# Kernel tuning notes

Measured on AMD Instinct MI355X. Metric: run time of the kernel, lower is better.

## Reference

```python
import jax, jax.numpy as jnp
import numpy as np

HIDDEN = 512
NUM_HEADS = 8
HEAD = HIDDEN // NUM_HEADS
TOP_K = 64
NEG = -1e9


def setup_inputs() -> dict:
    key = jax.random.key(0)
    ks = jax.random.split(key, 12)
    B, Q, S = 2, 2048, 4096
    sc = 0.02
    return {
        "main_input": jax.random.normal(ks[0], (B, Q, HIDDEN), jnp.float32),
        "side_input": jax.random.normal(ks[1], (S, HIDDEN), jnp.float32),
        "att_mask": jax.random.randint(ks[2], (B, Q, S), 0, 2, jnp.int32),
        "Wq": jax.random.normal(ks[3], (HIDDEN, HIDDEN), jnp.float32) * sc,
        "bq": jnp.zeros((HIDDEN,), jnp.float32),
        "Wk": jax.random.normal(ks[4], (HIDDEN, HIDDEN), jnp.float32) * sc,
        "bk": jnp.zeros((HIDDEN,), jnp.float32),
        "Wv": jax.random.normal(ks[5], (HIDDEN, HIDDEN), jnp.float32) * sc,
        "bv": jnp.zeros((HIDDEN,), jnp.float32),
        "Wo": jax.random.normal(ks[6], (HIDDEN, HIDDEN), jnp.float32) * sc,
        "bo": jnp.zeros((HIDDEN,), jnp.float32),
    }


def reference(main_input, side_input, att_mask, Wq, bq, Wk, bk, Wv, bv, Wo, bo):
    B, Qlen, _ = main_input.shape
    S = side_input.shape[0]
    # multi-head projections; side K/V shared across the whole batch
    q = (main_input @ Wq + bq).reshape(B, Qlen, NUM_HEADS, HEAD)
    k = (side_input @ Wk + bk).reshape(S, NUM_HEADS, HEAD)
    v = (side_input @ Wv + bv).reshape(S, NUM_HEADS, HEAD)
    # scores: [B, H, Q, S]
    scores = jnp.einsum("bqhd,khd->bhqk", q, k) / jnp.sqrt(jnp.asarray(HEAD, q.dtype))
    # attention mask (0 = masked)
    mask = att_mask[:, None, :, :].astype(scores.dtype)  # [B,1,Q,S]
    scores = scores + (1.0 - mask) * NEG
    # top-k restriction: keep only the TOP_K largest scores per query row
    thresh = jax.lax.top_k(scores, TOP_K)[0][..., -1:]  # kth largest
    scores = jnp.where(scores >= thresh, scores, NEG)
    probs = jax.nn.softmax(scores, axis=-1)
    ctx = jnp.einsum("bhqk,khd->bqhd", probs, v).reshape(B, Qlen, HIDDEN)
    return ctx @ Wo + bo
```

## Files before the change

kernel.cpp:

```cpp
#include <hip/hip_runtime.h>
#include <stdint.h>

typedef uint32_t u32;
typedef unsigned long long u64;

#define NEGV (-1e9f)
#define NCAND 16
#define LISTCAP 256
#define RSCALE 2048.0f
#define RINV   (1.0f / 2048.0f)
#define DELTA  4e-3f

typedef __attribute__((ext_vector_type(8))) _Float16 half8;
typedef __attribute__((ext_vector_type(4))) float f32x4;

__device__ __forceinline__ u32 f2ord(float f) {
  u32 x = __float_as_uint(f);
  return (x & 0x80000000u) ? ~x : (x | 0x80000000u);
}
__device__ __forceinline__ float ord2f(u32 u) {
  u32 x = (u & 0x80000000u) ? (u ^ 0x80000000u) : ~u;
  return __uint_as_float(x);
}

__device__ __forceinline__ void gl_lds16(const unsigned short* g, unsigned short* l) {
  __builtin_amdgcn_global_load_lds(
      (const __attribute__((address_space(1))) u32*)g,
      (__attribute__((address_space(3))) u32*)l, 16, 0, 0);
}

__global__ __launch_bounds__(256)
void pack_mask(const int* __restrict__ mask, u64* __restrict__ mbits) {
  int w = blockIdx.x * 256 + threadIdx.x;
  const int4* p = (const int4*)(mask + (size_t)w * 64);
  u64 bits = 0;
#pragma unroll
  for (int j = 0; j < 16; ++j) {
    int4 m = p[j];
    if (m.x) bits |= 1ull << (j * 4 + 0);
    if (m.y) bits |= 1ull << (j * 4 + 1);
    if (m.z) bits |= 1ull << (j * 4 + 2);
    if (m.w) bits |= 1ull << (j * 4 + 3);
  }
  mbits[w] = bits;
}

__global__ __launch_bounds__(256)
void gemm_bias(const float* __restrict__ A, const float* __restrict__ W,
               const float* __restrict__ bias, float* __restrict__ C) {
  __shared__ float As[16][68];
  __shared__ float Bs[16][64];
  const int tid = threadIdx.x;
  const int tx = tid & 15, ty = tid >> 4;
  const int n0 = blockIdx.x << 6, m0 = blockIdx.y << 6;
  float c[4][4] = {};
  for (int k0 = 0; k0 < 512; k0 += 16) {
    {
      const int row = tid >> 2, kp = (tid & 3) << 2;
      float4 av = *(const float4*)&A[(size_t)(m0 + row) * 512 + k0 + kp];
      As[kp + 0][row] = av.x;
      As[kp + 1][row] = av.y;
      As[kp + 2][row] = av.z;
      As[kp + 3][row] = av.w;
      const int kk = tid >> 4, np = (tid & 15) << 2;
      *(float4*)&Bs[kk][np] = *(const float4*)&W[(size_t)(k0 + kk) * 512 + n0 + np];
    }
    __syncthreads();
#pragma unroll
    for (int kk = 0; kk < 16; ++kk) {
      float4 a = *(const float4*)&As[kk][ty << 2];
      float4 b = *(const float4*)&Bs[kk][tx << 2];
      c[0][0] += a.x * b.x; c[0][1] += a.x * b.y; c[0][2] += a.x * b.z; c[0][3] += a.x * b.w;
      c[1][0] += a.y * b.x; c[1][1] += a.y * b.y; c[1][2] += a.y * b.z; c[1][3] += a.y * b.w;
      c[2][0] += a.z * b.x; c[2][1] += a.z * b.y; c[2][2] += a.z * b.z; c[2][3] += a.z * b.w;
      c[3][0] += a.w * b.x; c[3][1] += a.w * b.y; c[3][2] += a.w * b.z; c[3][3] += a.w * b.w;
    }
    __syncthreads();
  }
  float4 bv = *(const float4*)&bias[n0 + (tx << 2)];
#pragma unroll
  for (int i = 0; i < 4; ++i) {
    float4 o;
    o.x = c[i][0] + bv.x; o.y = c[i][1] + bv.y;
    o.z = c[i][2] + bv.z; o.w = c[i][3] + bv.w;
    *(float4*)&C[(size_t)(m0 + (ty << 2) + i) * 512 + n0 + (tx << 2)] = o;
  }
}

__global__ __launch_bounds__(256)
void gemm_bias_split(const float* __restrict__ A, const float* __restrict__ W,
                     const float* __restrict__ bias,
                     unsigned short* __restrict__ Ph, unsigned short* __restrict__ Pl,
                     float* __restrict__ Pf, int qsh) {
  __shared__ float As[16][68];
  __shared__ float Bs[16][64];
  const int tid = threadIdx.x;
  const int tx = tid & 15, ty = tid >> 4;
  const int n0 = blockIdx.x << 6, m0 = blockIdx.y << 6;
  float c[4][4] = {};
  for (int k0 = 0; k0 < 512; k0 += 16) {
    {
      const int row = tid >> 2, kp = (tid & 3) << 2;
      float4 av = *(const float4*)&A[(size_t)(m0 + row) * 512 + k0 + kp];
      As[kp + 0][row] = av.x;
      As[kp + 1][row] = av.y;
      As[kp + 2][row] = av.z;
      As[kp + 3][row] = av.w;
      const int kk = tid >> 4, np = (tid & 15) << 2;
      *(float4*)&Bs[kk][np] = *(const float4*)&W[(size_t)(k0 + kk) * 512 + n0 + np];
    }
    __syncthreads();
#pragma unroll
    for (int kk = 0; kk < 16; ++kk) {
      float4 a = *(const float4*)&As[kk][ty << 2];
      float4 b = *(const float4*)&Bs[kk][tx << 2];
      c[0][0] += a.x * b.x; c[0][1] += a.x * b.y; c[0][2] += a.x * b.z; c[0][3] += a.x * b.w;
      c[1][0] += a.y * b.x; c[1][1] += a.y * b.y; c[1][2] += a.y * b.z; c[1][3] += a.y * b.w;
      c[2][0] += a.z * b.x; c[2][1] += a.z * b.y; c[2][2] += a.z * b.z; c[2][3] += a.z * b.w;
      c[3][0] += a.w * b.x; c[3][1] += a.w * b.y; c[3][2] += a.w * b.z; c[3][3] += a.w * b.w;
    }
    __syncthreads();
  }
  float4 bv = *(const float4*)&bias[n0 + (tx << 2)];
  float bvv[4] = {bv.x, bv.y, bv.z, bv.w};
  const int h = blockIdx.x;
  const int QL = 1 << qsh;
#pragma unroll
  for (int i = 0; i < 4; ++i) {
    const int m = m0 + (ty << 2) + i;
    const size_t base =
        (((size_t)((m >> qsh) * 8 + h)) * QL + (m & (QL - 1))) * 64 + (tx << 2);
    u64 hb = 0, lb = 0;
    float fv[4];
#pragma unroll
    for (int j = 0; j < 4; ++j) {
      float val = c[i][j] + bvv[j];
      fv[j] = val;
      union { _Float16 f; unsigned short u; } ch, cl;
      ch.f = (_Float16)val;
      float hf = (float)ch.f;
      cl.f = (_Float16)((val - hf) * RSCALE);
      hb |= (u64)ch.u << (16 * j);
      lb |= (u64)cl.u << (16 * j);
    }
    float4 fo;
    fo.x = fv[0]; fo.y = fv[1]; fo.z = fv[2]; fo.w = fv[3];
    *(u64*)&Ph[base] = hb;
    *(u64*)&Pl[base] = lb;
    *(float4*)&Pf[base] = fo;
  }
}

__global__ __launch_bounds__(256, 2)
void score_mfma(const unsigned short* __restrict__ qh, const unsigned short* __restrict__ ql,
                const unsigned short* __restrict__ kh, const unsigned short* __restrict__ kl,
                const u64* __restrict__ mbits, float* __restrict__ sbuf,
                float* __restrict__ segmax, int sl0) {
  __shared__ alignas(16) unsigned short lds[4][128][64];
  const int sl = sl0 + blockIdx.z;
  const int b = sl >> 3, h = sl & 7;
  const int s0 = blockIdx.x << 7, q0 = blockIdx.y << 7;
  const int tid = threadIdx.x;
  const int lane = tid & 63, w = tid >> 6;

  const unsigned short* q0p = qh + ((size_t)sl * 2048 + q0) * 64;
  const unsigned short* q1p = ql + ((size_t)sl * 2048 + q0) * 64;
  const unsigned short* k0p = kh + ((size_t)h * 4096 + s0) * 64;
  const unsigned short* k1p = kl + ((size_t)h * 4096 + s0) * 64;

  {
    const int r8 = lane >> 3, pc = lane & 7;
#pragma unroll
    for (int u = 0; u < 4; ++u) {
      const int row = (w << 5) + (u << 3) + r8;
      const size_t src = (size_t)row * 64 + (size_t)((pc ^ (row & 7)) << 3);
      unsigned short* d0 = &lds[0][(w << 5) + (u << 3)][0];
      unsigned short* d1 = &lds[1][(w << 5) + (u << 3)][0];
      unsigned short* d2 = &lds[2][(w << 5) + (u << 3)][0];
      unsigned short* d3 = &lds[3][(w << 5) + (u << 3)][0];
      gl_lds16(q0p + src, d0);
      gl_lds16(q1p + src, d1);
      gl_lds16(k0p + src, d2);
      gl_lds16(k1p + src, d3);
    }
  }
  __syncthreads();

  const int r16 = lane & 15, g = lane >> 4;
  const int qw = (w >> 1) << 6;
  const int sw = (w & 1) << 6;

  f32x4 accB[4][4] = {};
  f32x4 accS[4][4] = {};
  half8 aH[2][4], bH[2][4], tX[2][4];

#define FRAG(p, rowbase, c_)                                                     \
  (*(const half8*)&lds[p][(rowbase) + r16][(((c_) ^ (((rowbase) + r16) & 7)) << 3)])

#pragma unroll
  for (int ks = 0; ks < 2; ++ks)
#pragma unroll
    for (int i = 0; i < 4; ++i) {
      aH[ks][i] = FRAG(0, qw + (i << 4), g + (ks << 2));
      bH[ks][i] = FRAG(2, sw + (i << 4), g + (ks << 2));
    }
#pragma unroll
  for (int ks = 0; ks < 2; ++ks)
#pragma unroll
    for (int i = 0; i < 4; ++i)
#pragma unroll
      for (int j = 0; j < 4; ++j)
        accB[i][j] = __builtin_amdgcn_mfma_f32_16x16x32_f16(aH[ks][i], bH[ks][j], accB[i][j], 0, 0, 0);
#pragma unroll
  for (int ks = 0; ks < 2; ++ks)
#pragma unroll
    for (int i = 0; i < 4; ++i)
      tX[ks][i] = FRAG(3, sw + (i << 4), g + (ks << 2));
#pragma unroll
  for (int ks = 0; ks < 2; ++ks)
#pragma unroll
    for (int i = 0; i < 4; ++i)
#pragma unroll
      for (int j = 0; j < 4; ++j)
        accS[i][j] = __builtin_amdgcn_mfma_f32_16x16x32_f16(aH[ks][i], tX[ks][j], accS[i][j], 0, 0, 0);
#pragma unroll
  for (int ks = 0; ks < 2; ++ks)
#pragma unroll
    for (int i = 0; i < 4; ++i)
      tX[ks][i] = FRAG(1, qw + (i << 4), g + (ks << 2));
#pragma unroll
  for (int ks = 0; ks < 2; ++ks)
#pragma unroll
    for (int i = 0; i < 4; ++i)
#pragma unroll
      for (int j = 0; j < 4; ++j)
        accS[i][j] = __builtin_amdgcn_mfma_f32_16x16x32_f16(tX[ks][i], bH[ks][j], accS[i][j], 0, 0, 0);
#undef FRAG

  const int sword = (s0 + sw) >> 6;
  const int sseg = (s0 + sw) >> 5;
#pragma unroll
  for (int i = 0; i < 4; ++i) {
#pragma unroll
    for (int r = 0; r < 4; ++r) {
      const int qg = q0 + qw + (i << 4) + (g << 2) + r;
      const u64 wm = mbits[((size_t)b * 2048 + qg) * 64 + sword];
      float s0v = (accB[i][0][r] + accS[i][0][r] * RINV) * 0.125f;
      float s1v = (accB[i][1][r] + accS[i][1][r] * RINV) * 0.125f;
      float s2v = (accB[i][2][r] + accS[i][2][r] * RINV) * 0.125f;
      float s3v = (accB[i][3][r] + accS[i][3][r] * RINV) * 0.125f;
      float v0 = ((wm >> (0 + r16)) & 1)  ? s0v : NEGV;
      float v1 = ((wm >> (16 + r16)) & 1) ? s1v : NEGV;
      float v2 = ((wm >> (32 + r16)) & 1) ? s2v : NEGV;
      float v3 = ((wm >> (48 + r16)) & 1) ? s3v : NEGV;
      float* rowp = sbuf + ((size_t)blockIdx.z * 2048 + qg) * 4096 + s0 + sw;
      rowp[r16] = v0;
      rowp[16 + r16] = v1;
      rowp[32 + r16] = v2;
      rowp[48 + r16] = v3;
      float m01 = fmaxf(v0, v1), m23 = fmaxf(v2, v3);
#pragma unroll
      for (int off = 8; off; off >>= 1) {
        m01 = fmaxf(m01, __shfl_xor(m01, off, 64));
        m23 = fmaxf(m23, __shfl_xor(m23, off, 64));
      }
      if (r16 == 0) {
        size_t sg = ((size_t)blockIdx.z * 2048 + qg) * 128 + sseg;
        segmax[sg] = m01;
        segmax[sg + 1] = m23;
      }
    }
  }
}

__global__ __launch_bounds__(256)
void topk_ctx_kernel(const float* __restrict__ sbuf, const float* __restrict__ segmax,
                     const float* __restrict__ vbuf,
                     const float* __restrict__ qF, const float* __restrict__ kF,
                     float* __restrict__ ctxbuf, int sl0) {
  const int sl = sl0 + blockIdx.y;
  const int b = sl >> 3, h = sl & 7;
  const int w = threadIdx.x >> 6, lane = threadIdx.x & 63;
  const int qi = (blockIdx.x << 2) + w;
  __shared__ u64 cand_lds[4][NCAND][64];
  __shared__ u64 list_lds[4][LISTCAP];
  __shared__ alignas(16) float qrow[4][64];
  u64* list = &list_lds[w][0];
  const u64 lmask_lt = (1ull << lane) - 1ull;

  const float* srow = sbuf + ((size_t)blockIdx.y * 2048 + qi) * 4096;

  qrow[w][lane] = qF[((size_t)sl * 2048 + qi) * 64 + lane];
  __syncthreads();

  float2 smv = *(const float2*)(segmax + ((size_t)blockIdx.y * 2048 + qi) * 128 + (lane << 1));
  u32 so0 = f2ord(smv.x), so1 = f2ord(smv.y);
  u32 mxo = so0 > so1 ? so0 : so1;
  u32 mno = so0 < so1 ? so0 : so1;
#pragma unroll
  for (int off = 32; off; off >>= 1) {
    u32 a = (u32)__shfl_xor((int)mxo, off, 64);
    u32 c = (u32)__shfl_xor((int)mno, off, 64);
    mxo = a > mxo ? a : mxo;
    mno = c < mno ? c : mno;
  }
  const float fm = ord2f(mxo);
  {
    u32 lo = mno, hi = mxo + 1;
    while (hi - lo > 1) {
      u32 mid = lo + ((hi - lo) >> 1);
      int c = __popcll(__ballot(so0 >= mid)) + __popcll(__ballot(so1 >= mid));
      if (c >= 64) lo = mid; else hi = mid;
    }
    mno = lo;
  }
  const u32 ordT = mno;
  const float TfD = ord2f(ordT) - DELTA;

  int cnt = 0;
  const float* lbase = srow + (lane << 6);
#pragma unroll
  for (int reg = 0; reg < 2; ++reg) {
    bool active = (reg == 0) ? (smv.x >= TfD) : (smv.y >= TfD);
    if (active) {
      const float* rb = lbase + (reg << 5);
      float4 v0 = *(const float4*)(rb + 0);
      float4 v1 = *(const float4*)(rb + 4);
      float4 v2 = *(const float4*)(rb + 8);
      float4 v3 = *(const float4*)(rb + 12);
      float4 v4 = *(const float4*)(rb + 16);
      float4 v5 = *(const float4*)(rb + 20);
      float4 v6 = *(const float4*)(rb + 24);
      float4 v7 = *(const float4*)(rb + 28);
      float xs[32] = {v0.x, v0.y, v0.z, v0.w, v1.x, v1.y, v1.z, v1.w,
                      v2.x, v2.y, v2.z, v2.w, v3.x, v3.y, v3.z, v3.w,
                      v4.x, v4.y, v4.z, v4.w, v5.x, v5.y, v5.z, v5.w,
                      v6.x, v6.y, v6.z, v6.w, v7.x, v7.y, v7.z, v7.w};
#pragma unroll
      for (int cc = 0; cc < 32; ++cc) {
        if (xs[cc] >= TfD) {
          if (cnt < NCAND) {
            int sidx = (lane << 6) + (reg << 5) + cc;
            cand_lds[w][cnt][lane] = ((u64)f2ord(xs[cc]) << 32) | (u32)sidx;
          }
          cnt++;
        }
      }
    }
  }
  const bool fb = (__ballot(cnt > NCAND) != 0ull);

  float esum = 0.f;
  int nsel = 0;
  bool meanpath = false;

  if (!fb) {
    const float* kb = kF + (size_t)h * 4096 * 64;
    u32 co[NCAND];
    u32 mymax = 0u, mymin = 0xFFFFFFFFu;
#pragma unroll
    for (int j = 0; j < NCAND; ++j) {
      if (j < cnt) {
        const u32 sidx = (u32)cand_lds[w][j][lane];
        const float* kr = kb + (size_t)sidx * 64;
        double acc = 0.0;
#pragma unroll 4
        for (int dq = 0; dq < 16; ++dq) {
          float4 kv = *(const float4*)(kr + (dq << 2));
          float4 qv = *(const float4*)&qrow[w][dq << 2];
          acc += (double)kv.x * (double)qv.x;
          acc += (double)kv.y * (double)qv.y;
          acc += (double)kv.z * (double)qv.z;
          acc += (double)kv.w * (double)qv.w;
        }
        float s = (float)(acc * 0.125);
        u32 o = f2ord(s);
        co[j] = o;
        mymax = o > mymax ? o : mymax;
        mymin = o < mymin ? o : mymin;
      } else {
        co[j] = 0u;
      }
    }
#pragma unroll
    for (int off = 32; off; off >>= 1) {
      u32 a = (u32)__shfl_xor((int)mymax, off, 64);
      u32 c = (u32)__shfl_xor((int)mymin, off, 64);
      mymax = a > mymax ? a : mymax;
      mymin = c < mymin ? c : mymin;
    }
    const float fmr = ord2f(mymax);
    u32 lo = mymin, hi = mymax + 1;
    while (hi - lo > 1) {
      u32 mid = lo + ((hi - lo) >> 1);
      int c = 0;
#pragma unroll
      for (int j = 0; j < NCAND; ++j)
        c += __popcll(__ballot(co[j] >= mid));
      if (c >= 64) lo = mid; else hi = mid;
    }
    int base = 0;
#pragma unroll
    for (int j = 0; j < NCAND; ++j) {
      bool pred = (j < cnt) && (co[j] >= lo);
      u64 m = __ballot(pred);
      int ofs = base + __popcll(m & lmask_lt);
      if (pred && ofs < LISTCAP) {
        u32 sidx = (u32)cand_lds[w][j][lane];
        float ev = __expf(ord2f(co[j]) - fmr);
        list[ofs] = ((u64)sidx << 32) | (u64)__float_as_uint(ev);
        esum += ev;
      }
      base += (int)__popcll(m);
    }
    nsel = base < LISTCAP ? base : LISTCAP;
  } else {
    u32 lo = ordT, hi = mxo + 1;
    while (hi - lo > 1) {
      u32 mid = lo + ((hi - lo) >> 1);
      float midf = ord2f(mid);
      int c = 0;
      for (int j = 0; j < 16; ++j) {
        float4 v = *(const float4*)(srow + (j << 8) + (lane << 2));
        c += __popcll(__ballot(v.x >= midf)) + __popcll(__ballot(v.y >= midf)) +
             __popcll(__ballot(v.z >= midf)) + __popcll(__ballot(v.w >= midf));
      }
      if (c >= 64) lo = mid; else hi = mid;
    }
    const float thrf = ord2f(lo);
    int base = 0;
    for (int j = 0; j < 16; ++j) {
      float4 v = *(const float4*)(srow + (j << 8) + (lane << 2));
      float xs[4] = {v.x, v.y, v.z, v.w};
#pragma unroll
      for (int cpos = 0; cpos < 4; ++cpos) {
        float x = xs[cpos];
        bool pred = (x >= thrf) && (x != NEGV);
        u64 m = __ballot(pred);
        int ofs = base + __popcll(m & lmask_lt);
        if (pred && ofs < LISTCAP) {
          int sidx = (j << 8) + (lane << 2) + cpos;
          float ev = __expf(x - fm);
          list[ofs] = ((u64)(u32)sidx << 32) | (u64)__float_as_uint(ev);
          esum += ev;
        }
        base += (int)__popcll(m);
      }
    }
    nsel = base < LISTCAP ? base : LISTCAP;
    if (base == 0) meanpath = true;
  }

#pragma unroll
  for (int off = 32; off; off >>= 1) esum += __shfl_xor(esum, off, 64);
  const float* vb = vbuf + h * 64 + lane;
  float outv;
  if (!meanpath) {
    const float rs = 1.0f / esum;
    int pad = (8 - (nsel & 7)) & 7;
    if (lane < pad && nsel + lane < LISTCAP) list[nsel + lane] = 0;
    int n8 = nsel + pad;
    if (n8 > LISTCAP) n8 = LISTCAP;
    float a0 = 0.f, a1 = 0.f, a2 = 0.f, a3 = 0.f;
    float a4 = 0.f, a5 = 0.f, a6 = 0.f, a7 = 0.f;
    for (int g = 0; g < n8; g += 8) {
      u64 p0 = list[g + 0], p1 = list[g + 1], p2 = list[g + 2], p3 = list[g + 3];
      u64 p4 = list[g + 4], p5 = list[g + 5], p6 = list[g + 6], p7 = list[g + 7];
      a0 += __uint_as_float((u32)p0) * vb[(size_t)(p0 >> 32) * 512];
      a1 += __uint_as_float((u32)p1) * vb[(size_t)(p1 >> 32) * 512];
      a2 += __uint_as_float((u32)p2) * vb[(size_t)(p2 >> 32) * 512];
      a3 += __uint_as_float((u32)p3) * vb[(size_t)(p3 >> 32) * 512];
      a4 += __uint_as_float((u32)p4) * vb[(size_t)(p4 >> 32) * 512];
      a5 += __uint_as_float((u32)p5) * vb[(size_t)(p5 >> 32) * 512];
      a6 += __uint_as_float((u32)p6) * vb[(size_t)(p6 >> 32) * 512];
      a7 += __uint_as_float((u32)p7) * vb[(size_t)(p7 >> 32) * 512];
    }
    outv = (((a0 + a1) + (a2 + a3)) + ((a4 + a5) + (a6 + a7))) * rs;
  } else {
    float acc = 0.f;
    for (int s = 0; s < 4096; ++s) acc += vb[(size_t)s * 512];
    outv = acc * (1.0f / 4096.0f);
  }
  ctxbuf[((size_t)(b * 2048 + qi)) * 512 + h * 64 + lane] = outv;
}

extern "C" void kernel_launch(void* const* d_in, const int* in_sizes, int n_in,
                              void* d_out, int out_size, void* d_ws, size_t ws_size,
                              hipStream_t stream) {
  const float* main_in = (const float*)d_in[0];
  const float* side_in = (const float*)d_in[1];
  const int*   mask    = (const int*)d_in[2];
  const float* Wq = (const float*)d_in[3];
  const float* bq = (const float*)d_in[4];
  const float* Wk = (const float*)d_in[5];
  const float* bk = (const float*)d_in[6];
  const float* Wv = (const float*)d_in[7];
  const float* bv = (const float*)d_in[8];
  const float* Wo = (const float*)d_in[9];
  const float* bo = (const float*)d_in[10];
  float* out = (float*)d_out;

  char* ws = (char*)d_ws;
  float* vbuf = (float*)(ws);
  float* ctxb = (float*)(ws + ((size_t)8 << 20));
  unsigned short* qhp = (unsigned short*)(ws + ((size_t)16 << 20));
  unsigned short* qlp = (unsigned short*)(ws + ((size_t)20 << 20));
  unsigned short* khp = (unsigned short*)(ws + ((size_t)24 << 20));
  unsigned short* klp = (unsigned short*)(ws + ((size_t)28 << 20));
  u64* mbits  = (u64*)(ws + ((size_t)32 << 20));
  float* qFp  = (float*)(ws + ((size_t)34 << 20));
  float* kFp  = (float*)(ws + ((size_t)42 << 20));
  const size_t base = (size_t)50 << 20;
  const size_t sliceb = (size_t)2048 * 4096 * 4;
  const size_t segb   = (size_t)2048 * 128 * 4;
  const size_t per = sliceb + segb;

  int nz = 1;
  if (ws_size > base) {
    size_t m = (ws_size - base) / per;
    if (m >= 1) nz = (int)(m > 4 ? 4 : m);
  }
  float* sbuf = (float*)(ws + base);
  float* smax = (float*)(ws + base + (size_t)nz * sliceb);

  pack_mask<<<1024, 256, 0, stream>>>(mask, mbits);
  gemm_bias_split<<<dim3(8, 64), 256, 0, stream>>>(main_in, Wq, bq, qhp, qlp, qFp, 11);
  gemm_bias_split<<<dim3(8, 64), 256, 0, stream>>>(side_in, Wk, bk, khp, klp, kFp, 12);
  gemm_bias  <<<dim3(8, 64), 256, 0, stream>>>(side_in, Wv, bv, vbuf);

  for (int sl0 = 0; sl0 < 16; sl0 += nz) {
    int z = nz < (16 - sl0) ? nz : (16 - sl0);
    score_mfma     <<<dim3(32, 16, z), 256, 0, stream>>>(qhp, qlp, khp, klp, mbits, sbuf, smax, sl0);
    topk_ctx_kernel<<<dim3(512, z), 256, 0, stream>>>(sbuf, smax, vbuf,
                                                      qFp, kFp, ctxb, sl0);
  }

  gemm_bias<<<dim3(8, 64), 256, 0, stream>>>(ctxb, Wo, bo, out);
}
```

Measured before the change: 826.8 us.

## Trim top-k candidate refinement: coarser threshold search, wave-max loop bounds, 16-bit LDS

The candidate buffer in LDS now holds only 16-bit key indices instead of packed 64-bit score+index words, which cuts LDS footprint and store traffic. The segment-max threshold bisection stops once the remaining interval is within 4096 ordinal units, saving ballot iterations. Candidate rescoring, bisection and list-building loops now break at the wave-wide maximum candidate count instead of always running NCAND iterations. The double-precision dot product is split into four independent accumulators to shorten the dependency chain. Risks: the coarser threshold admits more candidates and so raises the chance of taking the fallback path, and the multi-accumulator sum changes rounding slightly.

```diff
diff --git a/kernel.cpp b/kernel.cpp
--- a/kernel.cpp
+++ b/kernel.cpp
@@ -282,7 +282,7 @@
   const int b = sl >> 3, h = sl & 7;
   const int w = threadIdx.x >> 6, lane = threadIdx.x & 63;
   const int qi = (blockIdx.x << 2) + w;
-  __shared__ u64 cand_lds[4][NCAND][64];
+  __shared__ unsigned short cand_lds[4][NCAND][64];
   __shared__ u64 list_lds[4][LISTCAP];
   __shared__ alignas(16) float qrow[4][64];
   u64* list = &list_lds[w][0];
@@ -307,7 +307,7 @@
   const float fm = ord2f(mxo);
   {
     u32 lo = mno, hi = mxo + 1;
-    while (hi - lo > 1) {
+    while (hi - lo > 4096u) {
       u32 mid = lo + ((hi - lo) >> 1);
       int c = __popcll(__ballot(so0 >= mid)) + __popcll(__ballot(so1 >= mid));
       if (c >= 64) lo = mid; else hi = mid;
@@ -341,7 +341,7 @@
         if (xs[cc] >= TfD) {
           if (cnt < NCAND) {
             int sidx = (lane << 6) + (reg << 5) + cc;
-            cand_lds[w][cnt][lane] = ((u64)f2ord(xs[cc]) << 32) | (u32)sidx;
+            cand_lds[w][cnt][lane] = (unsigned short)sidx;
           }
           cnt++;
         }
@@ -349,6 +349,13 @@
     }
   }
   const bool fb = (__ballot(cnt > NCAND) != 0ull);
+  int mc = cnt;
+#pragma unroll
+  for (int off = 32; off; off >>= 1) {
+    int o = __shfl_xor(mc, off, 64);
+    mc = o > mc ? o : mc;
+  }
+  if (mc > NCAND) mc = NCAND;
 
   float esum = 0.f;
   int nsel = 0;
@@ -360,20 +367,21 @@
     u32 mymax = 0u, mymin = 0xFFFFFFFFu;
 #pragma unroll
     for (int j = 0; j < NCAND; ++j) {
+      if (j >= mc) break;
       if (j < cnt) {
         const u32 sidx = (u32)cand_lds[w][j][lane];
         const float* kr = kb + (size_t)sidx * 64;
-        double acc = 0.0;
-#pragma unroll 4
+        double a0 = 0.0, a1 = 0.0, a2 = 0.0, a3 = 0.0;
+#pragma unroll
         for (int dq = 0; dq < 16; ++dq) {
           float4 kv = *(const float4*)(kr + (dq << 2));
           float4 qv = *(const float4*)&qrow[w][dq << 2];
-          acc += (double)kv.x * (double)qv.x;
-          acc += (double)kv.y * (double)qv.y;
-          acc += (double)kv.z * (double)qv.z;
-          acc += (double)kv.w * (double)qv.w;
+          a0 += (double)kv.x * (double)qv.x;
+          a1 += (double)kv.y * (double)qv.y;
+          a2 += (double)kv.z * (double)qv.z;
+          a3 += (double)kv.w * (double)qv.w;
         }
-        float s = (float)(acc * 0.125);
+        float s = (float)(((a0 + a1) + (a2 + a3)) * 0.125);
         u32 o = f2ord(s);
         co[j] = o;
         mymax = o > mymax ? o : mymax;
@@ -383,6 +391,9 @@
       }
     }
 #pragma unroll
+    for (int j = 0; j < NCAND; ++j)
+      if (j >= mc) co[j] = 0u;
+#pragma unroll
     for (int off = 32; off; off >>= 1) {
       u32 a = (u32)__shfl_xor((int)mymax, off, 64);
       u32 c = (u32)__shfl_xor((int)mymin, off, 64);
@@ -395,13 +406,16 @@
       u32 mid = lo + ((hi - lo) >> 1);
       int c = 0;
 #pragma unroll
-      for (int j = 0; j < NCAND; ++j)
+      for (int j = 0; j < NCAND; ++j) {
+        if (j >= mc) break;
         c += __popcll(__ballot(co[j] >= mid));
+      }
       if (c >= 64) lo = mid; else hi = mid;
     }
     int base = 0;
 #pragma unroll
     for (int j = 0; j < NCAND; ++j) {
+      if (j >= mc) break;
       bool pred = (j < cnt) && (co[j] >= lo);
       u64 m = __ballot(pred);
       int ofs = base + __popcll(m & lmask_lt);
```

Result: faster. 793.3 us (-4.1%).
